# Performance work log

Measured on AMD Instinct MI355X. Metric: run time of the kernel, lower is better.

Reference implementation:

```python
import math
import jax, jax.numpy as jnp
import numpy as np

B, N, ND, CD, H, L, T = 2, 384, 8, 16, 128, 4, 100

def silu(x):
    return x * jax.nn.sigmoid(x)

def mlp2(x, w1, b1, w2, b2):
    return silu(x @ w1 + b1) @ w2 + b2

def setup_inputs() -> dict:
    key = jax.random.key(0)
    ks = iter(jax.random.split(key, 80))
    def nrm(shape, scale=1.0):
        return jax.random.normal(next(ks), shape, jnp.float32) * scale
    def lin(fi, fo):
        s = 1.0 / np.sqrt(fi)
        return nrm((fi, fo), s), nrm((fo,), s)
    def stack_lin(fi, fo):
        ws, bs = zip(*[lin(fi, fo) for _ in range(L)])
        return jnp.stack(ws), jnp.stack(bs)
    inp = {}
    inp['node_features'] = nrm((B, N, ND))
    inp['positions'] = nrm((B, N, 2))
    inp['mask'] = jnp.ones((B, N), jnp.float32)
    inp['condition'] = nrm((B, CD))
    inp['targets'] = nrm((B, 4))
    inp['property_weights'] = jax.random.uniform(next(ks), (4,), jnp.float32)
    inp['feature_noise'] = nrm((B, N, ND))
    inp['position_noise'] = nrm((B, N, 2))
    inp['timesteps'] = jax.random.randint(next(ks), (B,), 0, T)
    inp['time_w1'], inp['time_b1'] = lin(H, H)
    inp['time_w2'], inp['time_b2'] = lin(H, H)
    inp['cond_w1'], inp['cond_b1'] = lin(CD, H)
    inp['cond_w2'], inp['cond_b2'] = lin(H, H)
    inp['nodep_w1'], inp['nodep_b1'] = lin(ND + 2, H)
    inp['nodep_w2'], inp['nodep_b2'] = lin(H, H)
    inp['edge_w1'], inp['edge_b1'] = stack_lin(2 * H + 1, H)
    inp['edge_w2'], inp['edge_b2'] = stack_lin(H, H)
    inp['nodem_w1'], inp['nodem_b1'] = stack_lin(2 * H, H)
    inp['nodem_w2'], inp['nodem_b2'] = stack_lin(H, H)
    inp['feat_w1'], inp['feat_b1'] = lin(H, H)
    inp['feat_w2'], inp['feat_b2'] = lin(H, ND)
    inp['pos_w1'], inp['pos_b1'] = lin(H, H)
    inp['pos_w2'], inp['pos_b2'] = lin(H, 2)
    inp['prop_w1'], inp['prop_b1'] = lin(H, H)
    inp['prop_w2'], inp['prop_b2'] = lin(H, H // 2)
    inp['prop_w3'], inp['prop_b3'] = lin(H // 2, 4)
    return inp

def reference(node_features, positions, mask, condition, targets, property_weights,
              feature_noise, position_noise, timesteps,
              time_w1, time_b1, time_w2, time_b2,
              cond_w1, cond_b1, cond_w2, cond_b2,
              nodep_w1, nodep_b1, nodep_w2, nodep_b2,
              edge_w1, edge_b1, edge_w2, edge_b2,
              nodem_w1, nodem_b1, nodem_w2, nodem_b2,
              feat_w1, feat_b1, feat_w2, feat_b2,
              pos_w1, pos_b1, pos_w2, pos_b2,
              prop_w1, prop_b1, prop_w2, prop_b2, prop_w3, prop_b3):
    # diffusion schedule buffers
    betas = jnp.linspace(1e-4, 0.02, T)
    alpha_bars = jnp.cumprod(1.0 - betas)
    ab = alpha_bars[timesteps][:, None, None]
    nf = jnp.sqrt(ab) * node_features + jnp.sqrt(1.0 - ab) * feature_noise
    npos = jnp.sqrt(ab) * positions + jnp.sqrt(1.0 - ab) * position_noise
    # sinusoidal time embedding
    half = H // 2
    factor = math.log(10000.0) / (half - 1)
    freqs = jnp.exp(jnp.arange(half) * (-factor))
    te = timesteps.astype(jnp.float32)[:, None] * freqs[None, :]
    temb = jnp.concatenate([jnp.sin(te), jnp.cos(te)], -1)
    state = (mlp2(jnp.concatenate([nf, npos], -1), nodep_w1, nodep_b1, nodep_w2, nodep_b2)
             + mlp2(temb, time_w1, time_b1, time_w2, time_b2)[:, None, :]
             + mlp2(condition, cond_w1, cond_b1, cond_w2, cond_b2)[:, None, :])
    # pairwise distances (fixed across layers); eps for grad-safe sqrt at diagonal
    rel = npos[:, :, None, :] - npos[:, None, :, :]
    dist = jnp.sqrt(jnp.sum(rel * rel, -1) + 1e-12)  # [B,N,N]
    emask = mask[:, :, None] * mask[:, None, :]       # [B,N,N]
    denom = jnp.clip(emask.sum(2), 1.0)[..., None]    # [B,N,1]
    mask3 = mask[..., None]

    def layer(s, p):
        ew1, eb1, ew2, eb2, nw1, nb1, nw2, nb2 = p
        # split first edge-linear: cat([node_i, node_j, dist]) @ ew1
        ai = s @ ew1[:H]            # [B,N,H] (i contribution)
        aj = s @ ew1[H:2 * H]       # [B,N,H] (j contribution)
        h = silu(ai[:, :, None, :] + aj[:, None, :, :] + dist[..., None] * ew1[2 * H] + eb1)
        msg = (h @ ew2 + eb2) * emask[..., None]
        agg = msg.sum(2) / denom    # [B,N,H]
        upd = silu(s @ nw1[:H] + agg @ nw1[H:] + nb1) @ nw2 + nb2
        return s + upd * mask3, None

    state, _ = jax.lax.scan(layer, state,
                            (edge_w1, edge_b1, edge_w2, edge_b2,
                             nodem_w1, nodem_b1, nodem_w2, nodem_b2))
    pred_fn = mlp2(state, feat_w1, feat_b1, feat_w2, feat_b2)
    pred_pn = mlp2(state, pos_w1, pos_b1, pos_w2, pos_b2)
    gemb = (state * mask3).sum(1) / jnp.clip(mask.sum(1, keepdims=True), 1.0)
    props = silu(silu(gemb @ prop_w1 + prop_b1) @ prop_w2 + prop_b2) @ prop_w3 + prop_b3
    msum = jnp.clip(mask.sum(), 1.0)
    floss = (((pred_fn - feature_noise) ** 2) * mask3).sum() / msum
    ploss = (((pred_pn - position_noise) ** 2) * mask3).sum() / msum
    noise_loss = floss + ploss
    prop_loss = (((props - targets) ** 2) * property_weights).mean()
    total_loss = noise_loss + prop_loss
    return jnp.stack([noise_loss, prop_loss, total_loss])
```

## Files before the change

kernel.cpp:

```cpp
#include <hip/hip_runtime.h>
#include <math.h>

#define BB 2
#define NN 384
#define ND 8
#define CD 16
#define HH 128
#define LL 4
#define TT 100
#define TOTN (BB * NN)

__device__ __forceinline__ float silu_f(float x) {
    float s = 1.0f / (1.0f + __expf(-x));
    return x * s;
}

__global__ void k_prep(const float* __restrict__ mask, const float* __restrict__ condition,
                       const int* __restrict__ timesteps,
                       const float* __restrict__ time_w1, const float* __restrict__ time_b1,
                       const float* __restrict__ time_w2, const float* __restrict__ time_b2,
                       const float* __restrict__ cond_w1, const float* __restrict__ cond_b1,
                       const float* __restrict__ cond_w2, const float* __restrict__ cond_b2,
                       float* __restrict__ tc, float* __restrict__ scal, float* __restrict__ accums) {
    int b = blockIdx.x;
    int t = threadIdx.x;
    __shared__ float sh[HH];
    __shared__ float sh2[HH];
    __shared__ float shc[CD];
    __shared__ float red[HH];

    if (b == 0 && t < 2) accums[t] = 0.0f;

    int ts = timesteps[b];
    float ab = 1.0f;
    for (int k = 0; k <= ts; ++k) {
        float beta = 1e-4f + (0.02f - 1e-4f) * ((float)k / (float)(TT - 1));
        ab *= (1.0f - beta);
    }
    if (t == 0) {
        scal[b * 4 + 0] = sqrtf(ab);
        scal[b * 4 + 1] = sqrtf(1.0f - ab);
    }
    float m = 0.0f;
    for (int j = t; j < NN; j += HH) m += mask[b * NN + j];
    red[t] = m;
    __syncthreads();
    for (int s = 64; s > 0; s >>= 1) {
        if (t < s) red[t] += red[t + s];
        __syncthreads();
    }
    if (t == 0) scal[b * 4 + 2] = red[0];

    const int half = HH / 2;
    float factor = logf(10000.0f) / (float)(half - 1);
    float tf = (float)ts;
    float temb;
    if (t < half) temb = sinf(tf * __expf(-factor * (float)t));
    else          temb = cosf(tf * __expf(-factor * (float)(t - half)));
    sh[t] = temb;
    if (t < CD) shc[t] = condition[b * CD + t];
    __syncthreads();

    float acc = time_b1[t];
    for (int k = 0; k < HH; ++k) acc += sh[k] * time_w1[k * HH + t];
    sh2[t] = silu_f(acc);
    __syncthreads();
    float acc2 = time_b2[t];
    for (int k = 0; k < HH; ++k) acc2 += sh2[k] * time_w2[k * HH + t];
    float acc3 = cond_b1[t];
    for (int k = 0; k < CD; ++k) acc3 += shc[k] * cond_w1[k * HH + t];
    __syncthreads();
    sh[t] = silu_f(acc3);
    __syncthreads();
    float acc4 = cond_b2[t];
    for (int k = 0; k < HH; ++k) acc4 += sh[k] * cond_w2[k * HH + t];

    tc[b * HH + t] = acc2 + acc4;
}

__global__ __launch_bounds__(256) void k_node_init(
    const float* __restrict__ node_features, const float* __restrict__ positions,
    const float* __restrict__ feature_noise, const float* __restrict__ position_noise,
    const float* __restrict__ nodep_w1, const float* __restrict__ nodep_b1,
    const float* __restrict__ nodep_w2, const float* __restrict__ nodep_b2,
    const float* __restrict__ tc, const float* __restrict__ scal,
    const float* __restrict__ ew1_0, const float* __restrict__ eb1_0,
    float* __restrict__ state, float* __restrict__ npos,
    float* __restrict__ ai0, float* __restrict__ aj0) {
    const int tid = threadIdx.x;
    const int t = tid & 127;
    const int g = tid >> 7;
    const int b0 = blockIdx.x * 4;
    const int b = b0 / NN;

    __shared__ __align__(16) float x[4][12];
    __shared__ __align__(16) float sh1[4][HH];
    __shared__ __align__(16) float sst[4][HH];
    __shared__ float sred[4][2][HH];

    if (tid < 40) {
        int n = tid / 10, c = tid % 10;
        int gn = b0 + n;
        float sab = scal[b * 4 + 0], s1ab = scal[b * 4 + 1];
        float v;
        if (c < ND) {
            v = sab * node_features[gn * ND + c] + s1ab * feature_noise[gn * ND + c];
        } else {
            int d = c - ND;
            v = sab * positions[gn * 2 + d] + s1ab * position_noise[gn * 2 + d];
            npos[gn * 2 + d] = v;
        }
        x[n][c] = v;
    }
    __syncthreads();

    for (int n = 2 * g; n <= 2 * g + 1; ++n) {
        float a = nodep_b1[t];
        #pragma unroll
        for (int k = 0; k < ND + 2; ++k) a += x[n][k] * nodep_w1[k * HH + t];
        sh1[n][t] = silu_f(a);
    }
    __syncthreads();

    {
        float a0 = 0, a1 = 0, a2 = 0, a3 = 0;
        const int k0 = g * 64;
        const float* wr = nodep_w2 + (size_t)k0 * HH + t;
        for (int kk = 0; kk < 64; kk += 4) {
            float w0 = wr[(kk + 0) * HH], w1 = wr[(kk + 1) * HH];
            float w2 = wr[(kk + 2) * HH], w3 = wr[(kk + 3) * HH];
            float4 s;
            s = *(const float4*)&sh1[0][k0 + kk]; a0 += s.x * w0 + s.y * w1 + s.z * w2 + s.w * w3;
            s = *(const float4*)&sh1[1][k0 + kk]; a1 += s.x * w0 + s.y * w1 + s.z * w2 + s.w * w3;
            s = *(const float4*)&sh1[2][k0 + kk]; a2 += s.x * w0 + s.y * w1 + s.z * w2 + s.w * w3;
            s = *(const float4*)&sh1[3][k0 + kk]; a3 += s.x * w0 + s.y * w1 + s.z * w2 + s.w * w3;
        }
        sred[0][g][t] = a0; sred[1][g][t] = a1; sred[2][g][t] = a2; sred[3][g][t] = a3;
    }
    __syncthreads();
    {
        float tcv = nodep_b2[t] + tc[b * HH + t];
        for (int n = 2 * g; n <= 2 * g + 1; ++n) {
            float st = sred[n][0][t] + sred[n][1][t] + tcv;
            state[(size_t)(b0 + n) * HH + t] = st;
            sst[n][t] = st;
        }
    }
    __syncthreads();

    {
        float a0 = 0, a1 = 0, a2 = 0, a3 = 0;
        const int k0 = g * 64;
        const float* wr = ew1_0 + (size_t)k0 * HH + t;
        for (int kk = 0; kk < 64; kk += 4) {
            float w0 = wr[(kk + 0) * HH], w1 = wr[(kk + 1) * HH];
            float w2 = wr[(kk + 2) * HH], w3 = wr[(kk + 3) * HH];
            float4 s;
            s = *(const float4*)&sst[0][k0 + kk]; a0 += s.x * w0 + s.y * w1 + s.z * w2 + s.w * w3;
            s = *(const float4*)&sst[1][k0 + kk]; a1 += s.x * w0 + s.y * w1 + s.z * w2 + s.w * w3;
            s = *(const float4*)&sst[2][k0 + kk]; a2 += s.x * w0 + s.y * w1 + s.z * w2 + s.w * w3;
            s = *(const float4*)&sst[3][k0 + kk]; a3 += s.x * w0 + s.y * w1 + s.z * w2 + s.w * w3;
        }
        sred[0][g][t] = a0; sred[1][g][t] = a1; sred[2][g][t] = a2; sred[3][g][t] = a3;
    }
    __syncthreads();
    for (int n = 2 * g; n <= 2 * g + 1; ++n)
        ai0[(size_t)(b0 + n) * HH + t] = sred[n][0][t] + sred[n][1][t] + eb1_0[t];
    __syncthreads();
    {
        float a0 = 0, a1 = 0, a2 = 0, a3 = 0;
        const int k0 = g * 64;
        const float* wr = ew1_0 + (size_t)(HH + k0) * HH + t;
        for (int kk = 0; kk < 64; kk += 4) {
            float w0 = wr[(kk + 0) * HH], w1 = wr[(kk + 1) * HH];
            float w2 = wr[(kk + 2) * HH], w3 = wr[(kk + 3) * HH];
            float4 s;
            s = *(const float4*)&sst[0][k0 + kk]; a0 += s.x * w0 + s.y * w1 + s.z * w2 + s.w * w3;
            s = *(const float4*)&sst[1][k0 + kk]; a1 += s.x * w0 + s.y * w1 + s.z * w2 + s.w * w3;
            s = *(const float4*)&sst[2][k0 + kk]; a2 += s.x * w0 + s.y * w1 + s.z * w2 + s.w * w3;
            s = *(const float4*)&sst[3][k0 + kk]; a3 += s.x * w0 + s.y * w1 + s.z * w2 + s.w * w3;
        }
        sred[0][g][t] = a0; sred[1][g][t] = a1; sred[2][g][t] = a2; sred[3][g][t] = a3;
    }
    __syncthreads();
    for (int n = 2 * g; n <= 2 * g + 1; ++n)
        aj0[(size_t)(b0 + n) * HH + t] = sred[n][0][t] + sred[n][1][t];
}

__global__ void k_dist(const float* __restrict__ npos, float* __restrict__ dist) {
    int idx = blockIdx.x * blockDim.x + threadIdx.x;
    if (idx >= BB * NN * NN) return;
    int b = idx / (NN * NN);
    int r = idx % (NN * NN);
    int i = r / NN, j = r % NN;
    float dx = npos[(b * NN + i) * 2 + 0] - npos[(b * NN + j) * 2 + 0];
    float dy = npos[(b * NN + i) * 2 + 1] - npos[(b * NN + j) * 2 + 1];
    dist[idx] = sqrtf(dx * dx + dy * dy + 1e-12f);
}

__global__ __launch_bounds__(256) void k_edge(
    const float* __restrict__ ai, const float* __restrict__ aj,
    const float* __restrict__ dist, const float* __restrict__ mask,
    const float* __restrict__ wd, float* __restrict__ Sp) {
    const int tid = threadIdx.x;
    const int t = tid & 127;
    const int g = tid >> 7;
    const int blk = blockIdx.x;
    const int p = blk >> 2, q = blk & 3;
    const int n0 = p * 2, n1 = p * 2 + 1;
    const int b = n0 / NN;
    const int jb = q * 96;

    __shared__ __align__(16) float4 sdm[96];
    __shared__ float sred[2][2][HH];

    for (int i = tid; i < 96; i += 256) {
        int j = jb + i;
        sdm[i] = make_float4(dist[(size_t)n0 * NN + j], dist[(size_t)n1 * NN + j],
                             mask[b * NN + j], 0.0f);
    }
    const float av0 = ai[(size_t)n0 * HH + t];
    const float av1 = ai[(size_t)n1 * HH + t];
    const float wdt = wd[t];
    __syncthreads();

    const float* pa = aj + ((size_t)b * NN + jb) * HH + t;
    float acc0 = 0.0f, acc1 = 0.0f;
    #pragma unroll 4
    for (int i = g; i < 96; i += 2) {
        float4 dm = sdm[i];
        float a = pa[(size_t)i * HH];
        float v0 = av0 + a + dm.x * wdt;
        float v1 = av1 + a + dm.y * wdt;
        acc0 = fmaf(dm.z, silu_f(v0), acc0);
        acc1 = fmaf(dm.z, silu_f(v1), acc1);
    }
    sred[0][g][t] = acc0;
    sred[1][g][t] = acc1;
    __syncthreads();
    if (g == 0) Sp[((size_t)q * TOTN + n0) * HH + t] = sred[0][0][t] + sred[0][1][t];
    else        Sp[((size_t)q * TOTN + n1) * HH + t] = sred[1][0][t] + sred[1][1][t];
}

template<bool LAST>
__global__ __launch_bounds__(512) void k_nodeup(
    const float* __restrict__ Sp, float* __restrict__ state,
    const float* __restrict__ mask, const float* __restrict__ scal,
    const float* __restrict__ ew2, const float* __restrict__ eb2,
    const float* __restrict__ nw1, const float* __restrict__ nb1,
    const float* __restrict__ nw2, const float* __restrict__ nb2,
    const float* __restrict__ ew1n, const float* __restrict__ eb1n,
    float* __restrict__ ai_out, float* __restrict__ aj_out,
    const float* __restrict__ fnoise, const float* __restrict__ pnoise,
    const float* __restrict__ fw1, const float* __restrict__ fb1,
    const float* __restrict__ fw2, const float* __restrict__ fb2,
    const float* __restrict__ pw1, const float* __restrict__ pb1,
    const float* __restrict__ pw2, const float* __restrict__ pb2,
    float* __restrict__ accums, float* __restrict__ gembp) {
    const int tid = threadIdx.x;
    const int t = tid & 127;
    const int g = tid >> 7;
    const int b0 = blockIdx.x * 2;
    const int b = b0 / NN;

    __shared__ __align__(16) float sS[2][HH];
    __shared__ __align__(16) float sst[2][HH];
    __shared__ __align__(16) float sagg[2][HH];
    __shared__ __align__(16) float sh[2][HH];
    __shared__ float sred[2][4][HH];
    __shared__ float lf, lp;

    if (tid < 2 * HH) {
        int n = tid >> 7, tt = tid & 127;
        int gn = b0 + n;
        sS[n][tt] = Sp[((size_t)0 * TOTN + gn) * HH + tt] + Sp[((size_t)1 * TOTN + gn) * HH + tt]
                  + Sp[((size_t)2 * TOTN + gn) * HH + tt] + Sp[((size_t)3 * TOTN + gn) * HH + tt];
        sst[n][tt] = state[(size_t)gn * HH + tt];
    }
    if (tid == 0) { lf = 0.0f; lp = 0.0f; }
    __syncthreads();

    {
        float a0 = 0, a1 = 0;
        const int k0 = g * 32;
        const float* wr = ew2 + (size_t)k0 * HH + t;
        for (int kk = 0; kk < 32; kk += 4) {
            float w0 = wr[(kk + 0) * HH], w1 = wr[(kk + 1) * HH];
            float w2 = wr[(kk + 2) * HH], w3 = wr[(kk + 3) * HH];
            float4 s;
            s = *(const float4*)&sS[0][k0 + kk]; a0 += s.x * w0 + s.y * w1 + s.z * w2 + s.w * w3;
            s = *(const float4*)&sS[1][k0 + kk]; a1 += s.x * w0 + s.y * w1 + s.z * w2 + s.w * w3;
        }
        sred[0][g][t] = a0; sred[1][g][t] = a1;
    }
    __syncthreads();
    if (g < 2) {
        const float msum = scal[b * 4 + 2];
        float mi = mask[b0 + g];
        float denom = fmaxf(mi * msum, 1.0f);
        float a = sred[g][0][t] + sred[g][1][t] + sred[g][2][t] + sred[g][3][t] + msum * eb2[t];
        sagg[g][t] = mi * a / denom;
    }
    __syncthreads();

    {
        float a0 = 0, a1 = 0;
        const int r0 = g * 64;
        const float* wr = nw1 + (size_t)r0 * HH + t;
        const float (*inp)[HH] = (g < 2) ? (const float (*)[HH])sst : (const float (*)[HH])sagg;
        const int rb = (g & 1) * 64;
        for (int kk = 0; kk < 64; kk += 4) {
            float w0 = wr[(kk + 0) * HH], w1 = wr[(kk + 1) * HH];
            float w2 = wr[(kk + 2) * HH], w3 = wr[(kk + 3) * HH];
            float4 s;
            s = *(const float4*)&inp[0][rb + kk]; a0 += s.x * w0 + s.y * w1 + s.z * w2 + s.w * w3;
            s = *(const float4*)&inp[1][rb + kk]; a1 += s.x * w0 + s.y * w1 + s.z * w2 + s.w * w3;
        }
        sred[0][g][t] = a0; sred[1][g][t] = a1;
    }
    __syncthreads();
    if (g < 2) sh[g][t] = silu_f(sred[g][0][t] + sred[g][1][t] + sred[g][2][t] + sred[g][3][t] + nb1[t]);
    __syncthreads();

    {
        float a0 = 0, a1 = 0;
        const int k0 = g * 32;
        const float* wr = nw2 + (size_t)k0 * HH + t;
        for (int kk = 0; kk < 32; kk += 4) {
            float w0 = wr[(kk + 0) * HH], w1 = wr[(kk + 1) * HH];
            float w2 = wr[(kk + 2) * HH], w3 = wr[(kk + 3) * HH];
            float4 s;
            s = *(const float4*)&sh[0][k0 + kk]; a0 += s.x * w0 + s.y * w1 + s.z * w2 + s.w * w3;
            s = *(const float4*)&sh[1][k0 + kk]; a1 += s.x * w0 + s.y * w1 + s.z * w2 + s.w * w3;
        }
        sred[0][g][t] = a0; sred[1][g][t] = a1;
    }
    __syncthreads();
    if (g < 2) {
        int gn = b0 + g;
        float mi = mask[gn];
        float ns = sst[g][t] + (sred[g][0][t] + sred[g][1][t] + sred[g][2][t] + sred[g][3][t] + nb2[t]) * mi;
        state[(size_t)gn * HH + t] = ns;
        sst[g][t] = ns;
    }
    __syncthreads();

    if (!LAST) {
        {
            float a0 = 0, a1 = 0;
            const int k0 = g * 32;
            const float* wr = ew1n + (size_t)k0 * HH + t;
            for (int kk = 0; kk < 32; kk += 4) {
                float w0 = wr[(kk + 0) * HH], w1 = wr[(kk + 1) * HH];
                float w2 = wr[(kk + 2) * HH], w3 = wr[(kk + 3) * HH];
                float4 s;
                s = *(const float4*)&sst[0][k0 + kk]; a0 += s.x * w0 + s.y * w1 + s.z * w2 + s.w * w3;
                s = *(const float4*)&sst[1][k0 + kk]; a1 += s.x * w0 + s.y * w1 + s.z * w2 + s.w * w3;
            }
            sred[0][g][t] = a0; sred[1][g][t] = a1;
        }
        __syncthreads();
        if (g < 2) ai_out[(size_t)(b0 + g) * HH + t] =
            sred[g][0][t] + sred[g][1][t] + sred[g][2][t] + sred[g][3][t] + eb1n[t];
        __syncthreads();
        {
            float a0 = 0, a1 = 0;
            const int k0 = g * 32;
            const float* wr = ew1n + (size_t)(HH + k0) * HH + t;
            for (int kk = 0; kk < 32; kk += 4) {
                float w0 = wr[(kk + 0) * HH], w1 = wr[(kk + 1) * HH];
                float w2 = wr[(kk + 2) * HH], w3 = wr[(kk + 3) * HH];
                float4 s;
                s = *(const float4*)&sst[0][k0 + kk]; a0 += s.x * w0 + s.y * w1 + s.z * w2 + s.w * w3;
                s = *(const float4*)&sst[1][k0 + kk]; a1 += s.x * w0 + s.y * w1 + s.z * w2 + s.w * w3;
            }
            sred[0][g][t] = a0; sred[1][g][t] = a1;
        }
        __syncthreads();
        if (g < 2) aj_out[(size_t)(b0 + g) * HH + t] =
            sred[g][0][t] + sred[g][1][t] + sred[g][2][t] + sred[g][3][t];
    } else {
        {
            float a0 = 0, a1 = 0;
            const int k0 = g * 32;
            const float* wr = fw1 + (size_t)k0 * HH + t;
            for (int kk = 0; kk < 32; kk += 4) {
                float w0 = wr[(kk + 0) * HH], w1 = wr[(kk + 1) * HH];
                float w2 = wr[(kk + 2) * HH], w3 = wr[(kk + 3) * HH];
                float4 s;
                s = *(const float4*)&sst[0][k0 + kk]; a0 += s.x * w0 + s.y * w1 + s.z * w2 + s.w * w3;
                s = *(const float4*)&sst[1][k0 + kk]; a1 += s.x * w0 + s.y * w1 + s.z * w2 + s.w * w3;
            }
            sred[0][g][t] = a0; sred[1][g][t] = a1;
        }
        __syncthreads();
        if (g < 2) sS[g][t] = silu_f(sred[g][0][t] + sred[g][1][t] + sred[g][2][t] + sred[g][3][t] + fb1[t]);
        __syncthreads();
        {
            float a0 = 0, a1 = 0;
            const int k0 = g * 32;
            const float* wr = pw1 + (size_t)k0 * HH + t;
            for (int kk = 0; kk < 32; kk += 4) {
                float w0 = wr[(kk + 0) * HH], w1 = wr[(kk + 1) * HH];
                float w2 = wr[(kk + 2) * HH], w3 = wr[(kk + 3) * HH];
                float4 s;
                s = *(const float4*)&sst[0][k0 + kk]; a0 += s.x * w0 + s.y * w1 + s.z * w2 + s.w * w3;
                s = *(const float4*)&sst[1][k0 + kk]; a1 += s.x * w0 + s.y * w1 + s.z * w2 + s.w * w3;
            }
            sred[0][g][t] = a0; sred[1][g][t] = a1;
        }
        __syncthreads();
        if (g < 2) sagg[g][t] = silu_f(sred[g][0][t] + sred[g][1][t] + sred[g][2][t] + sred[g][3][t] + pb1[t]);
        __syncthreads();

        if (tid < 128) {
            int n = tid >> 6, lane = tid & 63;
            int gn = b0 + n;
            float mi = mask[gn];
            if (lane < ND) {
                float o = fb2[lane];
                for (int k = 0; k < HH; ++k) o += sS[n][k] * fw2[k * ND + lane];
                float d = o - fnoise[(size_t)gn * ND + lane];
                atomicAdd(&lf, mi * d * d);
            } else if (lane < ND + 2) {
                int c = lane - ND;
                float o = pb2[c];
                for (int k = 0; k < HH; ++k) o += sagg[n][k] * pw2[k * 2 + c];
                float d = o - pnoise[(size_t)gn * 2 + c];
                atomicAdd(&lp, mi * d * d);
            }
        }
        if (g == 0) {
            float v = sst[0][t] * mask[b0] + sst[1][t] * mask[b0 + 1];
            gembp[(size_t)blockIdx.x * HH + t] = v;
        }
        __syncthreads();
        if (tid == 0) {
            atomicAdd(&accums[0], lf);
            atomicAdd(&accums[1], lp);
        }
    }
}

__global__ __launch_bounds__(256) void k_final(
    const float* __restrict__ gembp, const float* __restrict__ targets,
    const float* __restrict__ pweights,
    const float* __restrict__ w1, const float* __restrict__ b1,
    const float* __restrict__ w2, const float* __restrict__ b2,
    const float* __restrict__ w3, const float* __restrict__ b3,
    const float* __restrict__ accums, const float* __restrict__ scal,
    float* __restrict__ out) {
    const int tid = threadIdx.x;
    const int t = tid & 127;
    const int b = tid >> 7;
    __shared__ float g2[BB][HH], h1[BB][HH], h2[BB][64];
    __shared__ float pl;
    if (tid == 0) pl = 0.0f;

    float acc = 0.0f;
    const float* gp = gembp + (size_t)b * 192 * HH + t;
    #pragma unroll 8
    for (int r = 0; r < 192; ++r) acc += gp[(size_t)r * HH];
    g2[b][t] = acc / fmaxf(scal[b * 4 + 2], 1.0f);
    __syncthreads();

    float a = b1[t];
    for (int k = 0; k < HH; ++k) a += g2[b][k] * w1[k * HH + t];
    h1[b][t] = silu_f(a);
    __syncthreads();
    if (t < 64) {
        float a2 = b2[t];
        for (int k = 0; k < HH; ++k) a2 += h1[b][k] * w2[k * 64 + t];
        h2[b][t] = silu_f(a2);
    }
    __syncthreads();
    if (t < 4) {
        float o = b3[t];
        for (int k = 0; k < 64; ++k) o += h2[b][k] * w3[k * 4 + t];
        float d = o - targets[b * 4 + t];
        atomicAdd(&pl, d * d * pweights[t]);
    }
    __syncthreads();
    if (tid == 0) {
        float msumt = fmaxf(scal[0 * 4 + 2] + scal[1 * 4 + 2], 1.0f);
        float noise = (accums[0] + accums[1]) / msumt;
        float prop = pl / (float)(BB * 4);
        out[0] = noise;
        out[1] = prop;
        out[2] = noise + prop;
    }
}

extern "C" void kernel_launch(void* const* d_in, const int* in_sizes, int n_in,
                              void* d_out, int out_size, void* d_ws, size_t ws_size,
                              hipStream_t stream) {
    const float* node_features  = (const float*)d_in[0];
    const float* positions      = (const float*)d_in[1];
    const float* mask           = (const float*)d_in[2];
    const float* condition     = (const float*)d_in[3];
    const float* targets        = (const float*)d_in[4];
    const float* pweights       = (const float*)d_in[5];
    const float* feature_noise  = (const float*)d_in[6];
    const float* position_noise = (const float*)d_in[7];
    const int*   timesteps      = (const int*)d_in[8];
    const float* time_w1 = (const float*)d_in[9];
    const float* time_b1 = (const float*)d_in[10];
    const float* time_w2 = (const float*)d_in[11];
    const float* time_b2 = (const float*)d_in[12];
    const float* cond_w1 = (const float*)d_in[13];
    const float* cond_b1 = (const float*)d_in[14];
    const float* cond_w2 = (const float*)d_in[15];
    const float* cond_b2 = (const float*)d_in[16];
    const float* nodep_w1 = (const float*)d_in[17];
    const float* nodep_b1 = (const float*)d_in[18];
    const float* nodep_w2 = (const float*)d_in[19];
    const float* nodep_b2 = (const float*)d_in[20];
    const float* edge_w1 = (const float*)d_in[21];
    const float* edge_b1 = (const float*)d_in[22];
    const float* edge_w2 = (const float*)d_in[23];
    const float* edge_b2 = (const float*)d_in[24];
    const float* nodem_w1 = (const float*)d_in[25];
    const float* nodem_b1 = (const float*)d_in[26];
    const float* nodem_w2 = (const float*)d_in[27];
    const float* nodem_b2 = (const float*)d_in[28];
    const float* feat_w1 = (const float*)d_in[29];
    const float* feat_b1 = (const float*)d_in[30];
    const float* feat_w2 = (const float*)d_in[31];
    const float* feat_b2 = (const float*)d_in[32];
    const float* pos_w1 = (const float*)d_in[33];
    const float* pos_b1 = (const float*)d_in[34];
    const float* pos_w2 = (const float*)d_in[35];
    const float* pos_b2 = (const float*)d_in[36];
    const float* prop_w1 = (const float*)d_in[37];
    const float* prop_b1 = (const float*)d_in[38];
    const float* prop_w2 = (const float*)d_in[39];
    const float* prop_b2 = (const float*)d_in[40];
    const float* prop_w3 = (const float*)d_in[41];
    const float* prop_b3 = (const float*)d_in[42];

    float* ws = (float*)d_ws;
    float* npos   = ws;
    float* state  = npos + BB * NN * 2;
    float* dist   = state + TOTN * HH;
    float* aiA    = dist + (size_t)TOTN * NN;
    float* ajA    = aiA + TOTN * HH;
    float* aiB    = ajA + TOTN * HH;
    float* ajB    = aiB + TOTN * HH;
    float* Sp     = ajB + TOTN * HH;
    float* tc     = Sp + 4 * TOTN * HH;
    float* scal   = tc + BB * HH;
    float* accums = scal + BB * 4;
    float* gembp  = accums + 2;

    float* outp = (float*)d_out;

    k_prep<<<BB, HH, 0, stream>>>(mask, condition, timesteps,
                                  time_w1, time_b1, time_w2, time_b2,
                                  cond_w1, cond_b1, cond_w2, cond_b2,
                                  tc, scal, accums);
    k_node_init<<<TOTN / 4, 256, 0, stream>>>(node_features, positions, feature_noise, position_noise,
                                              nodep_w1, nodep_b1, nodep_w2, nodep_b2,
                                              tc, scal, edge_w1, edge_b1, state, npos, aiA, ajA);
    k_dist<<<(BB * NN * NN + 255) / 256, 256, 0, stream>>>(npos, dist);

    for (int l = 0; l < LL; ++l) {
        const float* ew1l = edge_w1 + (size_t)l * (2 * HH + 1) * HH;
        const float* wd   = ew1l + (size_t)(2 * HH) * HH;
        const float* ew2  = edge_w2 + (size_t)l * HH * HH;
        const float* eb2  = edge_b2 + (size_t)l * HH;
        const float* nw1  = nodem_w1 + (size_t)l * 2 * HH * HH;
        const float* nb1  = nodem_b1 + (size_t)l * HH;
        const float* nw2  = nodem_w2 + (size_t)l * HH * HH;
        const float* nb2  = nodem_b2 + (size_t)l * HH;
        const float* ew1n = edge_w1 + (size_t)(l + 1) * (2 * HH + 1) * HH;
        const float* eb1n = edge_b1 + (size_t)(l + 1) * HH;

        const float* ai_in = (l & 1) ? aiB : aiA;
        const float* aj_in = (l & 1) ? ajB : ajA;
        float* ai_out = (l & 1) ? aiA : aiB;
        float* aj_out = (l & 1) ? ajA : ajB;

        k_edge<<<TOTN / 2 * 4, 256, 0, stream>>>(ai_in, aj_in, dist, mask, wd, Sp);

        if (l < LL - 1) {
            k_nodeup<false><<<TOTN / 2, 512, 0, stream>>>(
                Sp, state, mask, scal, ew2, eb2, nw1, nb1, nw2, nb2, ew1n, eb1n,
                ai_out, aj_out,
                feature_noise, position_noise, feat_w1, feat_b1, feat_w2, feat_b2,
                pos_w1, pos_b1, pos_w2, pos_b2, accums, gembp);
        } else {
            k_nodeup<true><<<TOTN / 2, 512, 0, stream>>>(
                Sp, state, mask, scal, ew2, eb2, nw1, nb1, nw2, nb2, ew1n, eb1n,
                ai_out, aj_out,
                feature_noise, position_noise, feat_w1, feat_b1, feat_w2, feat_b2,
                pos_w1, pos_b1, pos_w2, pos_b2, accums, gembp);
        }
    }

    k_final<<<1, 256, 0, stream>>>(gembp, targets, pweights,
                                   prop_w1, prop_b1, prop_w2, prop_b2, prop_w3, prop_b3,
                                   accums, scal, outp);
}
```

Measured before the change: 320.1 us.

## Fuse entire forward pass into one cooperative persistent kernel with grid syncs

Replaces the sequence of separate kernels (prep, node init, distance, per-layer edge/node kernels, heads) with a single cooperative kernel of 384 blocks, each handling two nodes, using grid.sync between layers. It recomputes the time/condition embedding per block, keeps distances, state and aggregates in shared memory, and uses the linearity of the second edge MLP layer to sum silu activations before the matmul, avoiding the per-edge matmul. It relies on all 384 blocks being co-resident; if the cooperative launch fails it falls back to the old multi-kernel path. Grid-wide syncs and redundant per-block weight loads are added costs.

```diff
diff --git a/kernel.cpp b/kernel.cpp
--- a/kernel.cpp
+++ b/kernel.cpp
@@ -1,5 +1,8 @@
 #include <hip/hip_runtime.h>
+#include <hip/hip_cooperative_groups.h>
 #include <math.h>
+
+namespace cg = cooperative_groups;
 
 #define BB 2
 #define NN 384
@@ -13,6 +16,335 @@
 __device__ __forceinline__ float silu_f(float x) {
     float s = 1.0f / (1.0f + __expf(-x));
     return x * s;
+}
+
+struct MegaParams {
+    const float *node_features, *positions, *mask, *condition, *targets, *pweights,
+                *feature_noise, *position_noise;
+    const int   *timesteps;
+    const float *time_w1, *time_b1, *time_w2, *time_b2;
+    const float *cond_w1, *cond_b1, *cond_w2, *cond_b2;
+    const float *nodep_w1, *nodep_b1, *nodep_w2, *nodep_b2;
+    const float *edge_w1, *edge_b1, *edge_w2, *edge_b2;
+    const float *nodem_w1, *nodem_b1, *nodem_w2, *nodem_b2;
+    const float *feat_w1, *feat_b1, *feat_w2, *feat_b2;
+    const float *pos_w1, *pos_b1, *pos_w2, *pos_b2;
+    const float *prop_w1, *prop_b1, *prop_w2, *prop_b2, *prop_w3, *prop_b3;
+    float *npos, *ajA, *ajB, *gembp, *gemb, *accums, *out;
+};
+
+__global__ __launch_bounds__(256, 2) void k_mega(MegaParams P) {
+    cg::grid_group grid = cg::this_grid();
+    const int p   = blockIdx.x;
+    const int n0  = p * 2;
+    const int b   = (n0 >= NN) ? 1 : 0;
+    const int l0  = n0 - b * NN;
+    const int tid = threadIdx.x;
+    const int t   = tid & 127;
+    const int g   = tid >> 7;
+    const int ng  = n0 + g;
+
+    __shared__ __align__(16) float s_pos[NN * 2];
+    __shared__ float s_d[2][NN];
+    __shared__ float s_mask[NN];
+    __shared__ __align__(16) float s_ai[2][HH];
+    __shared__ __align__(16) float s_S[2][HH];
+    __shared__ __align__(16) float s_st[2][HH];
+    __shared__ __align__(16) float s_h[2][HH];
+    __shared__ __align__(16) float s_agg[2][HH];
+    __shared__ float s_red[2][2][HH];
+    __shared__ float s_x[2][12];
+    __shared__ float s_cond[CD];
+    __shared__ float s_lfp[2];
+    float* r256 = &s_red[0][0][0];
+
+    const int ts = P.timesteps[b];
+    float ab = 1.0f;
+    for (int k = 0; k <= ts; ++k) {
+        float beta = 1e-4f + (0.02f - 1e-4f) * ((float)k / (float)(TT - 1));
+        ab *= (1.0f - beta);
+    }
+    const float sab = sqrtf(ab), s1ab = sqrtf(1.0f - ab);
+
+    for (int j = tid; j < NN; j += 256) s_mask[j] = P.mask[b * NN + j];
+    if (tid < CD) s_cond[tid] = P.condition[b * CD + tid];
+    __syncthreads();
+    {
+        float m = 0.0f;
+        for (int j = tid; j < NN; j += 256) m += s_mask[j];
+        r256[tid] = m;
+        __syncthreads();
+        for (int s = 128; s > 0; s >>= 1) {
+            if (tid < s) r256[tid] += r256[tid + s];
+            __syncthreads();
+        }
+    }
+    const float msum = r256[0];
+    __syncthreads();
+    if (l0 == 0 && tid == 0) P.accums[2 + b] = msum;
+    if (p == 0 && tid < 2) P.accums[tid] = 0.0f;
+
+    if (tid < HH) {
+        const int half = HH / 2;
+        float factor = logf(10000.0f) / (float)(half - 1);
+        float tf = (float)ts;
+        s_S[0][tid] = (tid < half) ? sinf(tf * __expf(-factor * (float)tid))
+                                   : cosf(tf * __expf(-factor * (float)(tid - half)));
+    }
+    __syncthreads();
+    {
+        float pp = 0.0f;
+        const int k0 = g * 64;
+        for (int k = k0; k < k0 + 64; ++k) pp += s_S[0][k] * P.time_w1[k * HH + t];
+        s_red[0][g][t] = pp;
+    }
+    __syncthreads();
+    if (g == 0) s_h[0][t] = silu_f(s_red[0][0][t] + s_red[0][1][t] + P.time_b1[t]);
+    __syncthreads();
+    float p2 = 0.0f;
+    {
+        const int k0 = g * 64;
+        for (int k = k0; k < k0 + 64; ++k) p2 += s_h[0][k] * P.time_w2[k * HH + t];
+    }
+    if (g == 0) {
+        float c1 = P.cond_b1[t];
+        for (int k = 0; k < CD; ++k) c1 += s_cond[k] * P.cond_w1[k * HH + t];
+        s_S[0][t] = silu_f(c1);
+    }
+    s_red[0][g][t] = p2;
+    __syncthreads();
+    const float timeL2 = s_red[0][0][t] + s_red[0][1][t];
+    __syncthreads();
+    {
+        float p4 = 0.0f;
+        const int k0 = g * 64;
+        for (int k = k0; k < k0 + 64; ++k) p4 += s_S[0][k] * P.cond_w2[k * HH + t];
+        s_red[0][g][t] = p4;
+    }
+    __syncthreads();
+    const float tc = timeL2 + P.time_b2[t] + s_red[0][0][t] + s_red[0][1][t] + P.cond_b2[t];
+    __syncthreads();
+
+    if (tid < 20) {
+        int nn = tid / 10, c = tid % 10;
+        int gnn = n0 + nn;
+        float v;
+        if (c < ND) {
+            v = sab * P.node_features[gnn * ND + c] + s1ab * P.feature_noise[gnn * ND + c];
+        } else {
+            int d = c - ND;
+            v = sab * P.positions[gnn * 2 + d] + s1ab * P.position_noise[gnn * 2 + d];
+            P.npos[gnn * 2 + d] = v;
+        }
+        s_x[nn][c] = v;
+    }
+    __syncthreads();
+    {
+        float a = P.nodep_b1[t];
+        #pragma unroll
+        for (int k = 0; k < ND + 2; ++k) a += s_x[g][k] * P.nodep_w1[k * HH + t];
+        s_h[g][t] = silu_f(a);
+    }
+    __syncthreads();
+    {
+        float pp = 0.0f;
+        for (int k = 0; k < HH; k += 4) {
+            float4 s = *(const float4*)&s_h[g][k];
+            const float* wr = P.nodep_w2 + (size_t)k * HH + t;
+            pp += s.x * wr[0] + s.y * wr[HH] + s.z * wr[2 * HH] + s.w * wr[3 * HH];
+        }
+        s_st[g][t] = pp + P.nodep_b2[t] + tc;
+    }
+    __syncthreads();
+    {
+        float pa = P.edge_b1[t], pj = 0.0f;
+        for (int k = 0; k < HH; ++k) {
+            float sk = s_st[g][k];
+            pa += sk * P.edge_w1[k * HH + t];
+            pj += sk * P.edge_w1[(HH + k) * HH + t];
+        }
+        s_ai[g][t] = pa;
+        P.ajA[(size_t)ng * HH + t] = pj;
+    }
+
+    grid.sync();
+
+    for (int i = tid; i < NN * 2; i += 256) s_pos[i] = P.npos[(size_t)b * NN * 2 + i];
+    __syncthreads();
+    {
+        float x0 = s_pos[l0 * 2],       y0 = s_pos[l0 * 2 + 1];
+        float x1 = s_pos[(l0 + 1) * 2], y1 = s_pos[(l0 + 1) * 2 + 1];
+        for (int j = tid; j < NN; j += 256) {
+            float px = s_pos[j * 2], py = s_pos[j * 2 + 1];
+            float dx0 = x0 - px, dy0 = y0 - py;
+            float dx1 = x1 - px, dy1 = y1 - py;
+            s_d[0][j] = sqrtf(dx0 * dx0 + dy0 * dy0 + 1e-12f);
+            s_d[1][j] = sqrtf(dx1 * dx1 + dy1 * dy1 + 1e-12f);
+        }
+    }
+    __syncthreads();
+    const float mi   = s_mask[l0 + g];
+    const float deno = fmaxf(mi * msum, 1.0f);
+
+    for (int l = 0; l < LL; ++l) {
+        const float* ew1l = P.edge_w1 + (size_t)l * (2 * HH + 1) * HH;
+        const float* ew2  = P.edge_w2 + (size_t)l * HH * HH;
+        const float* eb2  = P.edge_b2 + (size_t)l * HH;
+        const float* nw1  = P.nodem_w1 + (size_t)l * 2 * HH * HH;
+        const float* nb1  = P.nodem_b1 + (size_t)l * HH;
+        const float* nw2  = P.nodem_w2 + (size_t)l * HH * HH;
+        const float* nb2  = P.nodem_b2 + (size_t)l * HH;
+        const float wdt = ew1l[(size_t)(2 * HH) * HH + t];
+        const float* ajin = (l & 1) ? P.ajB : P.ajA;
+
+        const float av0 = s_ai[0][t], av1 = s_ai[1][t];
+        float acc0 = 0.0f, acc1 = 0.0f;
+        {
+            const float* pa = ajin + (size_t)b * NN * HH + t;
+            #pragma unroll 4
+            for (int j = g; j < NN; j += 2) {
+                float a = pa[(size_t)j * HH];
+                float m = s_mask[j];
+                acc0 = fmaf(m, silu_f(av0 + a + s_d[0][j] * wdt), acc0);
+                acc1 = fmaf(m, silu_f(av1 + a + s_d[1][j] * wdt), acc1);
+            }
+        }
+        s_red[0][g][t] = acc0;
+        s_red[1][g][t] = acc1;
+        __syncthreads();
+        s_S[g][t] = s_red[g][0][t] + s_red[g][1][t];
+        __syncthreads();
+
+        {
+            float pp = 0.0f;
+            for (int k = 0; k < HH; k += 4) {
+                float4 s = *(const float4*)&s_S[g][k];
+                const float* wr = ew2 + (size_t)k * HH + t;
+                pp += s.x * wr[0] + s.y * wr[HH] + s.z * wr[2 * HH] + s.w * wr[3 * HH];
+            }
+            s_agg[g][t] = mi * (pp + msum * eb2[t]) / deno;
+        }
+        __syncthreads();
+
+        {
+            float pp = 0.0f;
+            for (int k = 0; k < HH; k += 4) {
+                float4 s = *(const float4*)&s_st[g][k];
+                const float* wr = nw1 + (size_t)k * HH + t;
+                pp += s.x * wr[0] + s.y * wr[HH] + s.z * wr[2 * HH] + s.w * wr[3 * HH];
+            }
+            for (int k = 0; k < HH; k += 4) {
+                float4 s = *(const float4*)&s_agg[g][k];
+                const float* wr = nw1 + (size_t)(HH + k) * HH + t;
+                pp += s.x * wr[0] + s.y * wr[HH] + s.z * wr[2 * HH] + s.w * wr[3 * HH];
+            }
+            s_h[g][t] = silu_f(pp + nb1[t]);
+        }
+        __syncthreads();
+
+        {
+            float pp = 0.0f;
+            for (int k = 0; k < HH; k += 4) {
+                float4 s = *(const float4*)&s_h[g][k];
+                const float* wr = nw2 + (size_t)k * HH + t;
+                pp += s.x * wr[0] + s.y * wr[HH] + s.z * wr[2 * HH] + s.w * wr[3 * HH];
+            }
+            s_st[g][t] = s_st[g][t] + (pp + nb2[t]) * mi;
+        }
+        __syncthreads();
+
+        if (l < LL - 1) {
+            const float* ew1n = P.edge_w1 + (size_t)(l + 1) * (2 * HH + 1) * HH;
+            const float* eb1n = P.edge_b1 + (size_t)(l + 1) * HH;
+            float pa = eb1n[t], pj = 0.0f;
+            for (int k = 0; k < HH; ++k) {
+                float sk = s_st[g][k];
+                pa += sk * ew1n[k * HH + t];
+                pj += sk * ew1n[(HH + k) * HH + t];
+            }
+            s_ai[g][t] = pa;
+            float* ajout = (l & 1) ? P.ajA : P.ajB;
+            ajout[(size_t)ng * HH + t] = pj;
+            grid.sync();
+        }
+    }
+
+    {
+        float pf = P.feat_b1[t], pq = P.pos_b1[t];
+        for (int k = 0; k < HH; k += 4) {
+            float4 s = *(const float4*)&s_st[g][k];
+            const float* wf = P.feat_w1 + (size_t)k * HH + t;
+            const float* wp = P.pos_w1 + (size_t)k * HH + t;
+            pf += s.x * wf[0] + s.y * wf[HH] + s.z * wf[2 * HH] + s.w * wf[3 * HH];
+            pq += s.x * wp[0] + s.y * wp[HH] + s.z * wp[2 * HH] + s.w * wp[3 * HH];
+        }
+        s_S[g][t] = silu_f(pf);
+        s_h[g][t] = silu_f(pq);
+        if (tid == 0) { s_lfp[0] = 0.0f; s_lfp[1] = 0.0f; }
+    }
+    __syncthreads();
+    if (t < ND) {
+        float o = P.feat_b2[t];
+        for (int k = 0; k < HH; ++k) o += s_S[g][k] * P.feat_w2[k * ND + t];
+        float d = o - P.feature_noise[(size_t)ng * ND + t];
+        atomicAdd(&s_lfp[0], mi * d * d);
+    } else if (t >= 64 && t < 66) {
+        int c = t - 64;
+        float o = P.pos_b2[c];
+        for (int k = 0; k < HH; ++k) o += s_h[g][k] * P.pos_w2[k * 2 + c];
+        float d = o - P.position_noise[(size_t)ng * 2 + c];
+        atomicAdd(&s_lfp[1], mi * d * d);
+    }
+    P.gembp[(size_t)ng * HH + t] = s_st[g][t] * mi;
+    __syncthreads();
+    if (tid == 0) {
+        atomicAdd(&P.accums[0], s_lfp[0]);
+        atomicAdd(&P.accums[1], s_lfp[1]);
+    }
+
+    grid.sync();
+
+    if (l0 == 0) {
+        float acc = 0.0f;
+        const float* gp = P.gembp + (size_t)b * NN * HH + t;
+        for (int r = g; r < NN; r += 2) acc += gp[(size_t)r * HH];
+        s_red[0][g][t] = acc;
+        __syncthreads();
+        if (g == 0) P.gemb[b * HH + t] = (s_red[0][0][t] + s_red[0][1][t]) / fmaxf(msum, 1.0f);
+    }
+
+    grid.sync();
+
+    if (p == 0) {
+        s_S[g][t] = P.gemb[g * HH + t];
+        if (tid == 0) s_lfp[0] = 0.0f;
+        __syncthreads();
+        float a = P.prop_b1[t];
+        for (int k = 0; k < HH; ++k) a += s_S[g][k] * P.prop_w1[k * HH + t];
+        s_h[g][t] = silu_f(a);
+        __syncthreads();
+        if (t < 64) {
+            float a2 = P.prop_b2[t];
+            for (int k = 0; k < HH; ++k) a2 += s_h[g][k] * P.prop_w2[k * 64 + t];
+            s_agg[g][t] = silu_f(a2);
+        }
+        __syncthreads();
+        if (t < 4) {
+            float o = P.prop_b3[t];
+            for (int k = 0; k < 64; ++k) o += s_agg[g][k] * P.prop_w3[k * 4 + t];
+            float d = o - P.targets[g * 4 + t];
+            atomicAdd(&s_lfp[0], d * d * P.pweights[t]);
+        }
+        __syncthreads();
+        if (tid == 0) {
+            float msumt = fmaxf(P.accums[2] + P.accums[3], 1.0f);
+            float noise = (P.accums[0] + P.accums[1]) / msumt;
+            float prop  = s_lfp[0] / (float)(BB * 4);
+            P.out[0] = noise;
+            P.out[1] = prop;
+            P.out[2] = noise + prop;
+        }
+    }
 }
 
 __global__ void k_prep(const float* __restrict__ mask, const float* __restrict__ condition,
@@ -497,50 +829,63 @@
     const float* node_features  = (const float*)d_in[0];
     const float* positions      = (const float*)d_in[1];
     const float* mask           = (const float*)d_in[2];
-    const float* condition     = (const float*)d_in[3];
+    const float* condition      = (const float*)d_in[3];
     const float* targets        = (const float*)d_in[4];
     const float* pweights       = (const float*)d_in[5];
     const float* feature_noise  = (const float*)d_in[6];
     const float* position_noise = (const float*)d_in[7];
     const int*   timesteps      = (const int*)d_in[8];
-    const float* time_w1 = (const float*)d_in[9];
-    const float* time_b1 = (const float*)d_in[10];
-    const float* time_w2 = (const float*)d_in[11];
-    const float* time_b2 = (const float*)d_in[12];
-    const float* cond_w1 = (const float*)d_in[13];
-    const float* cond_b1 = (const float*)d_in[14];
-    const float* cond_w2 = (const float*)d_in[15];
-    const float* cond_b2 = (const float*)d_in[16];
-    const float* nodep_w1 = (const float*)d_in[17];
-    const float* nodep_b1 = (const float*)d_in[18];
-    const float* nodep_w2 = (const float*)d_in[19];
-    const float* nodep_b2 = (const float*)d_in[20];
-    const float* edge_w1 = (const float*)d_in[21];
-    const float* edge_b1 = (const float*)d_in[22];
-    const float* edge_w2 = (const float*)d_in[23];
-    const float* edge_b2 = (const float*)d_in[24];
-    const float* nodem_w1 = (const float*)d_in[25];
-    const float* nodem_b1 = (const float*)d_in[26];
-    const float* nodem_w2 = (const float*)d_in[27];
-    const float* nodem_b2 = (const float*)d_in[28];
-    const float* feat_w1 = (const float*)d_in[29];
-    const float* feat_b1 = (const float*)d_in[30];
-    const float* feat_w2 = (const float*)d_in[31];
-    const float* feat_b2 = (const float*)d_in[32];
-    const float* pos_w1 = (const float*)d_in[33];
-    const float* pos_b1 = (const float*)d_in[34];
-    const float* pos_w2 = (const float*)d_in[35];
-    const float* pos_b2 = (const float*)d_in[36];
-    const float* prop_w1 = (const float*)d_in[37];
-    const float* prop_b1 = (const float*)d_in[38];
-    const float* prop_w2 = (const float*)d_in[39];
-    const float* prop_b2 = (const float*)d_in[40];
-    const float* prop_w3 = (const float*)d_in[41];
-    const float* prop_b3 = (const float*)d_in[42];
+    const float* time_w1 = (const float*)d_in[9];   const float* time_b1 = (const float*)d_in[10];
+    const float* time_w2 = (const float*)d_in[11];  const float* time_b2 = (const float*)d_in[12];
+    const float* cond_w1 = (const float*)d_in[13];  const float* cond_b1 = (const float*)d_in[14];
+    const float* cond_w2 = (const float*)d_in[15];  const float* cond_b2 = (const float*)d_in[16];
+    const float* nodep_w1 = (const float*)d_in[17]; const float* nodep_b1 = (const float*)d_in[18];
+    const float* nodep_w2 = (const float*)d_in[19]; const float* nodep_b2 = (const float*)d_in[20];
+    const float* edge_w1 = (const float*)d_in[21];  const float* edge_b1 = (const float*)d_in[22];
+    const float* edge_w2 = (const float*)d_in[23];  const float* edge_b2 = (const float*)d_in[24];
+    const float* nodem_w1 = (const float*)d_in[25]; const float* nodem_b1 = (const float*)d_in[26];
+    const float* nodem_w2 = (const float*)d_in[27]; const float* nodem_b2 = (const float*)d_in[28];
+    const float* feat_w1 = (const float*)d_in[29];  const float* feat_b1 = (const float*)d_in[30];
+    const float* feat_w2 = (const float*)d_in[31];  const float* feat_b2 = (const float*)d_in[32];
+    const float* pos_w1 = (const float*)d_in[33];   const float* pos_b1 = (const float*)d_in[34];
+    const float* pos_w2 = (const float*)d_in[35];   const float* pos_b2 = (const float*)d_in[36];
+    const float* prop_w1 = (const float*)d_in[37];  const float* prop_b1 = (const float*)d_in[38];
+    const float* prop_w2 = (const float*)d_in[39];  const float* prop_b2 = (const float*)d_in[40];
+    const float* prop_w3 = (const float*)d_in[41];  const float* prop_b3 = (const float*)d_in[42];
 
     float* ws = (float*)d_ws;
-    float* npos   = ws;
-    float* state  = npos + BB * NN * 2;
+    float* outp = (float*)d_out;
+
+    MegaParams P;
+    P.node_features = node_features; P.positions = positions; P.mask = mask;
+    P.condition = condition; P.targets = targets; P.pweights = pweights;
+    P.feature_noise = feature_noise; P.position_noise = position_noise;
+    P.timesteps = timesteps;
+    P.time_w1 = time_w1; P.time_b1 = time_b1; P.time_w2 = time_w2; P.time_b2 = time_b2;
+    P.cond_w1 = cond_w1; P.cond_b1 = cond_b1; P.cond_w2 = cond_w2; P.cond_b2 = cond_b2;
+    P.nodep_w1 = nodep_w1; P.nodep_b1 = nodep_b1; P.nodep_w2 = nodep_w2; P.nodep_b2 = nodep_b2;
+    P.edge_w1 = edge_w1; P.edge_b1 = edge_b1; P.edge_w2 = edge_w2; P.edge_b2 = edge_b2;
+    P.nodem_w1 = nodem_w1; P.nodem_b1 = nodem_b1; P.nodem_w2 = nodem_w2; P.nodem_b2 = nodem_b2;
+    P.feat_w1 = feat_w1; P.feat_b1 = feat_b1; P.feat_w2 = feat_w2; P.feat_b2 = feat_b2;
+    P.pos_w1 = pos_w1; P.pos_b1 = pos_b1; P.pos_w2 = pos_w2; P.pos_b2 = pos_b2;
+    P.prop_w1 = prop_w1; P.prop_b1 = prop_b1; P.prop_w2 = prop_w2; P.prop_b2 = prop_b2;
+    P.prop_w3 = prop_w3; P.prop_b3 = prop_b3;
+    P.npos   = ws;
+    P.ajA    = P.npos + TOTN * 2;
+    P.ajB    = P.ajA + TOTN * HH;
+    P.gembp  = P.ajB + TOTN * HH;
+    P.gemb   = P.gembp + TOTN * HH;
+    P.accums = P.gemb + BB * HH;
+    P.out    = outp;
+
+    void* args[] = { &P };
+    hipError_t err = hipLaunchCooperativeKernel((const void*)k_mega, dim3(TOTN / 2), dim3(256),
+                                                args, 0, stream);
+    if (err == hipSuccess) return;
+
+    float* fb     = P.accums + 4;
+    float* npos   = fb;
+    float* state  = npos + TOTN * 2;
     float* dist   = state + TOTN * HH;
     float* aiA    = dist + (size_t)TOTN * NN;
     float* ajA    = aiA + TOTN * HH;
@@ -551,8 +896,6 @@
     float* scal   = tc + BB * HH;
     float* accums = scal + BB * 4;
     float* gembp  = accums + 2;
-
-    float* outp = (float*)d_out;
 
     k_prep<<<BB, HH, 0, stream>>>(mask, condition, timesteps,
                                   time_w1, time_b1, time_w2, time_b2,
```

Measured after the change: 697.3 us. 2.18x slower.
